# Performance work log

Measured on AMD Instinct MI355X. Metric: run time of the kernel, lower is better.

## Reference

```python
import jax, jax.numpy as jnp
import numpy as np

L, E, H, FF = 6, 768, 4, 3072
D = E // H
SCALE = float(E) ** -0.5  # note: source scales by embedding_size**-0.5, not head_dim
EPS = 1e-5


def layernorm(x, scale, bias):
    mu = jnp.mean(x, axis=-1, keepdims=True)
    var = jnp.mean((x - mu) ** 2, axis=-1, keepdims=True)
    return (x - mu) * jax.lax.rsqrt(var + EPS) * scale + bias


def setup_inputs() -> dict:
    key = jax.random.key(0)
    ks = jax.random.split(key, 16)
    s = 0.02
    inp = {
        "hidden_states": jax.random.normal(ks[0], (8, 1024, E), dtype=jnp.float32),
        "ln1_scale": jnp.ones((L, E), jnp.float32),
        "ln1_bias": jnp.zeros((L, E), jnp.float32),
        "wq": jax.random.normal(ks[1], (L, E, E), jnp.float32) * s,
        "wk": jax.random.normal(ks[2], (L, E, E), jnp.float32) * s,
        "wv": jax.random.normal(ks[3], (L, E, E), jnp.float32) * s,
        "wo": jax.random.normal(ks[4], (L, E, E), jnp.float32) * s,
        "bo": jnp.zeros((L, E), jnp.float32),
        "ln2_scale": jnp.ones((L, E), jnp.float32),
        "ln2_bias": jnp.zeros((L, E), jnp.float32),
        "w1": jax.random.normal(ks[5], (L, FF, E), jnp.float32) * s,
        "b1": jnp.zeros((L, FF), jnp.float32),
        "w2": jax.random.normal(ks[6], (L, E, FF), jnp.float32) * s,
        "b2": jnp.zeros((L, E), jnp.float32),
    }
    return inp


def _encoder(x, ln1_scale, ln1_bias, wq, wk, wv, wo, bo, ln2_scale, ln2_bias, w1, b1, w2, b2):
    B, S, _ = x.shape
    for i in range(L):
        h = layernorm(x, ln1_scale[i], ln1_bias[i])
        # torch Linear: y = x @ W.T
        q = (h @ wq[i].T).reshape(B, H, S, D)  # non-standard head split (reshape, no transpose) per source
        k = (h @ wk[i].T).reshape(B, H, S, D)
        v = (h @ wv[i].T).reshape(B, H, S, D)
        scores = jnp.einsum("bhsd,bhtd->bhst", q, k) * SCALE  # full SxS materialized, as in source
        attn = jax.nn.softmax(scores, axis=-1)
        o = jnp.einsum("bhst,bhtd->bhsd", attn, v)
        o = o.transpose(0, 2, 1, 3).reshape(B, S, E)
        x = x + (o @ wo[i].T + bo[i])
        h = layernorm(x, ln2_scale[i], ln2_bias[i])
        h = jax.nn.gelu(h @ w1[i].T + b1[i], approximate=False)  # nn.GELU default = exact erf
        x = x + (h @ w2[i].T + b2[i])  # dropout is identity in eval
    return x


def reference(hidden_states, ln1_scale, ln1_bias, wq, wk, wv, wo, bo, ln2_scale, ln2_bias, w1, b1, w2, b2):
    return _encoder(hidden_states, ln1_scale, ln1_bias, wq, wk, wv, wo, bo, ln2_scale, ln2_bias, w1, b1, w2, b2)
```

## Files before the change

kernel.cpp:

```cpp
#include <hip/hip_runtime.h>
#include <math.h>

typedef __attribute__((ext_vector_type(8))) __bf16 bf16x8;
typedef __attribute__((ext_vector_type(4))) __bf16 bf16x4;
typedef __attribute__((ext_vector_type(2))) __bf16 bf16x2;
typedef __attribute__((ext_vector_type(4))) float f32x4;

#define MFMA_BF16 __builtin_amdgcn_mfma_f32_16x16x32_bf16

constexpr int LAY = 6, E = 768, HH = 4, DH = 192, FF = 3072, BB = 8, SS = 1024, MM = 8192;
constexpr float ATT_SCALE = 0.03608439182435161f;

__device__ __forceinline__ void gl2lds16(const void* g, void* l) {
    __builtin_amdgcn_global_load_lds(
        (const __attribute__((address_space(1))) void*)g,
        (__attribute__((address_space(3))) void*)l, 16, 0, 0);
}

struct Cast6 {
    const float* src[6];
    __bf16* dst[6];
    int cum4[7];
};

__global__ __launch_bounds__(256) void cast6_kernel(Cast6 c, int total4) {
    int stride = gridDim.x * 256;
    for (int i = blockIdx.x * 256 + threadIdx.x; i < total4; i += stride) {
        int rgn = 0;
#pragma unroll
        for (int k = 1; k < 6; ++k) rgn += (i >= c.cum4[k]) ? 1 : 0;
        int off = i - c.cum4[rgn];
        f32x4 v = ((const f32x4*)c.src[rgn])[off];
        bf16x4 o;
        o[0] = (__bf16)v[0]; o[1] = (__bf16)v[1]; o[2] = (__bf16)v[2]; o[3] = (__bf16)v[3];
        ((bf16x4*)c.dst[rgn])[off] = o;
    }
}

__global__ __launch_bounds__(256) void ln_kernel(const float* __restrict__ x,
                                                 const float* __restrict__ gamma,
                                                 const float* __restrict__ beta,
                                                 __bf16* __restrict__ out) {
    size_t row = blockIdx.x;
    const float* xr = x + row * E;
    int t = threadIdx.x;
    float v0 = xr[t], v1 = xr[t + 256], v2 = xr[t + 512];
    float s = v0 + v1 + v2;
    float q = v0 * v0 + v1 * v1 + v2 * v2;
#pragma unroll
    for (int m = 1; m < 64; m <<= 1) { s += __shfl_xor(s, m); q += __shfl_xor(q, m); }
    __shared__ float red[8];
    int w = t >> 6;
    if ((t & 63) == 0) { red[w] = s; red[4 + w] = q; }
    __syncthreads();
    s = red[0] + red[1] + red[2] + red[3];
    q = red[4] + red[5] + red[6] + red[7];
    float mu = s * (1.0f / E);
    float var = q * (1.0f / E) - mu * mu;
    float rs = rsqrtf(var + 1e-5f);
    __bf16* orow = out + row * E;
    orow[t]       = (__bf16)((v0 - mu) * rs * gamma[t]       + beta[t]);
    orow[t + 256] = (__bf16)((v1 - mu) * rs * gamma[t + 256] + beta[t + 256]);
    orow[t + 512] = (__bf16)((v2 - mu) * rs * gamma[t + 512] + beta[t + 512]);
}

template <int EPI>
__global__ __launch_bounds__(256) void gemm_bt(
    const __bf16* __restrict__ A,
    const __bf16* __restrict__ B0, const __bf16* __restrict__ B1, const __bf16* __restrict__ B2,
    void* __restrict__ O0, void* __restrict__ O1, void* __restrict__ O2,
    const float* __restrict__ bias, int M, int N, int K) {
    __shared__ __bf16 smA[128 * 64];
    __shared__ __bf16 smB[128 * 64];
    int z = blockIdx.z;
    const __bf16* Bw = (z == 0) ? B0 : (z == 1) ? B1 : B2;
    void* Out = (z == 0) ? O0 : (z == 1) ? O1 : O2;
    int t = threadIdx.x;
    int w = t >> 6, lane = t & 63, b4 = lane >> 4, r = lane & 15;
    int mbase = blockIdx.y * 128, nbase = blockIdx.x * 128;
    int wm = (w >> 1) * 64, wn = (w & 1) * 64;
    const f32x4 fz = {0.f, 0.f, 0.f, 0.f};
    f32x4 acc[4][4];
#pragma unroll
    for (int a1 = 0; a1 < 4; ++a1)
#pragma unroll
        for (int a2 = 0; a2 < 4; ++a2) acc[a1][a2] = fz;
    const __bf16* Ap = A + (size_t)mbase * K;
    const __bf16* Bp = Bw + (size_t)nbase * K;
    int nk = K >> 6;
    for (int kt = 0; kt < nk; ++kt) {
        int k0 = kt * 64;
#pragma unroll
        for (int i = 0; i < 4; ++i) {
            int c = i * 256 + t;
            int row = c >> 3, ch = c & 7;
            int ldsoff = (i * 256 + w * 64) * 8;
            gl2lds16(Ap + (size_t)row * K + k0 + ch * 8, (void*)(smA + ldsoff));
            gl2lds16(Bp + (size_t)row * K + k0 + ch * 8, (void*)(smB + ldsoff));
        }
        __syncthreads();
#pragma unroll
        for (int ks = 0; ks < 2; ++ks) {
            bf16x8 af[4], bfr[4];
#pragma unroll
            for (int mi = 0; mi < 4; ++mi)
                af[mi] = *(const bf16x8*)(smA + (wm + mi * 16 + r) * 64 + ks * 32 + b4 * 8);
#pragma unroll
            for (int ni = 0; ni < 4; ++ni)
                bfr[ni] = *(const bf16x8*)(smB + (wn + ni * 16 + r) * 64 + ks * 32 + b4 * 8);
#pragma unroll
            for (int mi = 0; mi < 4; ++mi)
#pragma unroll
                for (int ni = 0; ni < 4; ++ni)
                    acc[mi][ni] = MFMA_BF16(af[mi], bfr[ni], acc[mi][ni], 0, 0, 0);
        }
        __syncthreads();
    }
#pragma unroll
    for (int mi = 0; mi < 4; ++mi) {
#pragma unroll
        for (int ni = 0; ni < 4; ++ni) {
            int col = nbase + wn + ni * 16 + r;
#pragma unroll
            for (int j = 0; j < 4; ++j) {
                int rowi = mbase + wm + mi * 16 + b4 * 4 + j;
                float v = acc[mi][ni][j];
                if constexpr (EPI == 0) {
                    ((__bf16*)Out)[(size_t)rowi * N + col] = (__bf16)v;
                } else if constexpr (EPI == 1) {
                    v += bias[col];
                    float g = 0.5f * v * (1.0f + erff(v * 0.70710678118654752f));
                    ((__bf16*)Out)[(size_t)rowi * N + col] = (__bf16)g;
                } else {
                    float* X = (float*)Out;
                    X[(size_t)rowi * N + col] += v + bias[col];
                }
            }
        }
    }
}

__global__ __launch_bounds__(256) void vtrans_kernel(const __bf16* __restrict__ v,
                                                     __bf16* __restrict__ vt) {
    __shared__ __bf16 tile[64 * 72];
    int bh = blockIdx.y;
    int si = blockIdx.x / 3, di = blockIdx.x % 3;
    int t = threadIdx.x;
    const __bf16* src = v + (size_t)bh * (SS * DH) + (size_t)(si * 64) * DH + di * 64;
#pragma unroll
    for (int i = 0; i < 2; ++i) {
        int c = i * 256 + t;
        int sl = c >> 3, dc = c & 7;
        *(bf16x8*)(tile + sl * 72 + dc * 8) = *(const bf16x8*)(src + (size_t)sl * DH + dc * 8);
    }
    __syncthreads();
    __bf16* dst = vt + ((size_t)bh * DH + di * 64) * SS + si * 64;
#pragma unroll
    for (int i = 0; i < 2; ++i) {
        int c = i * 256 + t;
        int dl = c >> 3, sc = c & 7;
        bf16x8 o;
#pragma unroll
        for (int e = 0; e < 8; ++e) o[e] = tile[(sc * 8 + e) * 72 + dl];
        *(bf16x8*)(dst + (size_t)dl * SS + sc * 8) = o;
    }
}

__global__ __launch_bounds__(256) void attn_kernel(const __bf16* __restrict__ qp,
                                                   const __bf16* __restrict__ kp,
                                                   const __bf16* __restrict__ vtp,
                                                   __bf16* __restrict__ ao) {
    __shared__ __bf16 smK[64 * 192];
    __shared__ __bf16 smVt[192 * 64];
    __shared__ __bf16 smP[4 * 16 * 72];
    int qt = blockIdx.x, h = blockIdx.y, b = blockIdx.z;
    int t = threadIdx.x, w = t >> 6, lane = t & 63, b4 = lane >> 4, r = lane & 15;
    size_t base = (size_t)b * (SS * E) + (size_t)h * (SS * DH);
    const __bf16* Q = qp + base;
    const __bf16* Kg = kp + base;
    const __bf16* VtG = vtp + (size_t)(b * HH + h) * DH * SS;
    int q0 = qt * 64 + w * 16;
    bf16x8 qf[6];
#pragma unroll
    for (int ks = 0; ks < 6; ++ks)
        qf[ks] = *(const bf16x8*)(Q + (size_t)(q0 + r) * DH + ks * 32 + b4 * 8);
    const f32x4 fz = {0.f, 0.f, 0.f, 0.f};
    f32x4 oacc[12];
#pragma unroll
    for (int i = 0; i < 12; ++i) oacc[i] = fz;
    float m_r[4], l_r[4];
#pragma unroll
    for (int j = 0; j < 4; ++j) { m_r[j] = -1e30f; l_r[j] = 0.f; }
    __bf16* smPw = smP + w * (16 * 72);

    for (int kt = 0; kt < 16; ++kt) {
        const __bf16* Ks = Kg + (size_t)kt * 64 * DH;
#pragma unroll
        for (int i = 0; i < 6; ++i) {
            int c = i * 256 + t;
            int row = c / 24, cc = c - row * 24;
            int scc = (cc & 0x18) | ((cc ^ row) & 7);
            gl2lds16(Ks + (size_t)row * DH + scc * 8,
                     (void*)(smK + (i * 256 + w * 64) * 8));
        }
#pragma unroll
        for (int i = 0; i < 6; ++i) {
            int c = i * 256 + t;
            int row = c >> 3, cc = c & 7;
            int scc = cc ^ (row & 7);
            gl2lds16(VtG + (size_t)row * SS + kt * 64 + scc * 8,
                     (void*)(smVt + (i * 256 + w * 64) * 8));
        }
        __syncthreads();
        f32x4 sc[4];
#pragma unroll
        for (int nt = 0; nt < 4; ++nt) sc[nt] = fz;
#pragma unroll
        for (int ks = 0; ks < 6; ++ks) {
#pragma unroll
            for (int nt = 0; nt < 4; ++nt) {
                int cc = ks * 4 + b4;
                int ccs = (cc & 0x18) | ((cc ^ r) & 7);
                bf16x8 kf = *(const bf16x8*)(smK + (nt * 16 + r) * 192 + ccs * 8);
                sc[nt] = MFMA_BF16(qf[ks], kf, sc[nt], 0, 0, 0);
            }
        }
#pragma unroll
        for (int nt = 0; nt < 4; ++nt) sc[nt] *= ATT_SCALE;
        float alpha[4];
#pragma unroll
        for (int j = 0; j < 4; ++j) {
            float mx = fmaxf(fmaxf(sc[0][j], sc[1][j]), fmaxf(sc[2][j], sc[3][j]));
#pragma unroll
            for (int msk = 1; msk < 16; msk <<= 1) mx = fmaxf(mx, __shfl_xor(mx, msk));
            float mn = fmaxf(m_r[j], mx);
            alpha[j] = __expf(m_r[j] - mn);
            m_r[j] = mn;
            float p0 = __expf(sc[0][j] - mn);
            float p1 = __expf(sc[1][j] - mn);
            float p2 = __expf(sc[2][j] - mn);
            float p3 = __expf(sc[3][j] - mn);
            sc[0][j] = p0; sc[1][j] = p1; sc[2][j] = p2; sc[3][j] = p3;
            float ps = p0 + p1 + p2 + p3;
#pragma unroll
            for (int msk = 1; msk < 16; msk <<= 1) ps += __shfl_xor(ps, msk);
            l_r[j] = l_r[j] * alpha[j] + ps;
        }
        {
            f32x4 a4 = {alpha[0], alpha[1], alpha[2], alpha[3]};
#pragma unroll
            for (int i = 0; i < 12; ++i) oacc[i] *= a4;
        }
#pragma unroll
        for (int nt = 0; nt < 4; ++nt)
#pragma unroll
            for (int j = 0; j < 4; ++j)
                smPw[(b4 * 4 + j) * 72 + nt * 16 + r] = (__bf16)sc[nt][j];
        __asm__ volatile("s_waitcnt lgkmcnt(0)" ::: "memory");
#pragma unroll
        for (int kt2 = 0; kt2 < 2; ++kt2) {
            bf16x8 pa = *(const bf16x8*)(smPw + r * 72 + kt2 * 32 + b4 * 8);
#pragma unroll
            for (int nt = 0; nt < 12; ++nt) {
                int ccs = (kt2 * 4 + b4) ^ (r & 7);
                bf16x8 vf = *(const bf16x8*)(smVt + (nt * 16 + r) * 64 + ccs * 8);
                oacc[nt] = MFMA_BF16(pa, vf, oacc[nt], 0, 0, 0);
            }
        }
        __syncthreads();
    }
    float inv[4];
#pragma unroll
    for (int j = 0; j < 4; ++j) inv[j] = 1.0f / l_r[j];
    __bf16* obase = ao + (size_t)b * (SS * E);
#pragma unroll
    for (int nt = 0; nt < 12; ++nt)
#pragma unroll
        for (int j = 0; j < 4; ++j) {
            int srow = q0 + b4 * 4 + j;
            obase[(size_t)srow * E + h * DH + nt * 16 + r] = (__bf16)(oacc[nt][j] * inv[j]);
        }
}

extern "C" void kernel_launch(void* const* d_in, const int* in_sizes, int n_in,
                              void* d_out, int out_size, void* d_ws, size_t ws_size,
                              hipStream_t stream) {
    const float* hs   = (const float*)d_in[0];
    const float* ln1s = (const float*)d_in[1];
    const float* ln1b = (const float*)d_in[2];
    const float* wq   = (const float*)d_in[3];
    const float* wk   = (const float*)d_in[4];
    const float* wv   = (const float*)d_in[5];
    const float* wo   = (const float*)d_in[6];
    const float* bo   = (const float*)d_in[7];
    const float* ln2s = (const float*)d_in[8];
    const float* ln2b = (const float*)d_in[9];
    const float* w1   = (const float*)d_in[10];
    const float* b1   = (const float*)d_in[11];
    const float* w2   = (const float*)d_in[12];
    const float* b2   = (const float*)d_in[13];
    float* X = (float*)d_out;

    char* ws = (char*)d_ws;
    size_t off = 0;
    auto alloc = [&](size_t bytes) {
        char* p = ws + off;
        off += (bytes + 255) & ~(size_t)255;
        return p;
    };
    __bf16* wq_b = (__bf16*)alloc((size_t)E * E * 2);
    __bf16* wk_b = (__bf16*)alloc((size_t)E * E * 2);
    __bf16* wv_b = (__bf16*)alloc((size_t)E * E * 2);
    __bf16* wo_b = (__bf16*)alloc((size_t)E * E * 2);
    __bf16* w1_b = (__bf16*)alloc((size_t)FF * E * 2);
    __bf16* w2_b = (__bf16*)alloc((size_t)FF * E * 2);
    __bf16* h_b  = (__bf16*)alloc((size_t)MM * E * 2);
    char* U = alloc((size_t)MM * FF * 2);
    const size_t SLOT = (size_t)MM * E * 2;
    __bf16* q_b  = (__bf16*)U;
    __bf16* k_b  = (__bf16*)(U + SLOT);
    __bf16* v_b  = (__bf16*)(U + 2 * SLOT);
    __bf16* vt_b = (__bf16*)(U + 3 * SLOT);
    __bf16* a_b  = (__bf16*)(U + 2 * SLOT);
    __bf16* f_b  = (__bf16*)U;

    hipMemcpyAsync(d_out, hs, (size_t)MM * E * 4, hipMemcpyDeviceToDevice, stream);

    for (int i = 0; i < LAY; ++i) {
        Cast6 c;
        c.src[0] = wq + (size_t)i * E * E;  c.dst[0] = wq_b;
        c.src[1] = wk + (size_t)i * E * E;  c.dst[1] = wk_b;
        c.src[2] = wv + (size_t)i * E * E;  c.dst[2] = wv_b;
        c.src[3] = wo + (size_t)i * E * E;  c.dst[3] = wo_b;
        c.src[4] = w1 + (size_t)i * FF * E; c.dst[4] = w1_b;
        c.src[5] = w2 + (size_t)i * FF * E; c.dst[5] = w2_b;
        int n4[6] = {E * E / 4, E * E / 4, E * E / 4, E * E / 4, FF * E / 4, FF * E / 4};
        c.cum4[0] = 0;
        for (int k = 0; k < 6; ++k) c.cum4[k + 1] = c.cum4[k] + n4[k];
        int total4 = c.cum4[6];
        cast6_kernel<<<1024, 256, 0, stream>>>(c, total4);

        ln_kernel<<<MM, 256, 0, stream>>>(X, ln1s + (size_t)i * E, ln1b + (size_t)i * E, h_b);

        gemm_bt<0><<<dim3(E / 128, MM / 128, 3), 256, 0, stream>>>(
            h_b, wq_b, wk_b, wv_b, q_b, k_b, v_b, nullptr, MM, E, E);

        vtrans_kernel<<<dim3(48, 32), 256, 0, stream>>>(v_b, vt_b);

        attn_kernel<<<dim3(SS / 64, HH, BB), 256, 0, stream>>>(q_b, k_b, vt_b, a_b);

        gemm_bt<2><<<dim3(E / 128, MM / 128, 1), 256, 0, stream>>>(
            a_b, wo_b, wo_b, wo_b, X, X, X, bo + (size_t)i * E, MM, E, E);

        ln_kernel<<<MM, 256, 0, stream>>>(X, ln2s + (size_t)i * E, ln2b + (size_t)i * E, h_b);

        gemm_bt<1><<<dim3(FF / 128, MM / 128, 1), 256, 0, stream>>>(
            h_b, w1_b, w1_b, w1_b, f_b, f_b, f_b, b1 + (size_t)i * FF, MM, FF, E);

        gemm_bt<2><<<dim3(E / 128, MM / 128, 1), 256, 0, stream>>>(
            f_b, w2_b, w2_b, w2_b, X, X, X, b2 + (size_t)i * E, MM, E, FF);
    }
}
```

Measured before the change: 2.158 ms.

## Replace 128x128 GEMM with 256x256 multi-stage pipelined MFMA kernel

The GEMM kernel now uses 256x256 output tiles with 512 threads and a 4-slot LDS ring buffer filled by async global-to-LDS loads, with explicit vmcnt waits. This replaces the single-buffered load/sync/compute loop. It also adds an XOR swizzle on LDS columns to avoid bank conflicts, remaps block IDs so neighbouring tiles land together, and raises MFMA priority with s_setprio. The larger tiles sharply cut the block count for the N=768 GEMMs, to 96 blocks for the Wo and W2 projections, which can leave many compute units idle.

```diff
diff --git a/kernel.cpp b/kernel.cpp
--- a/kernel.cpp
+++ b/kernel.cpp
@@ -65,65 +65,108 @@
 }
 
 template <int EPI>
-__global__ __launch_bounds__(256) void gemm_bt(
+__global__ __launch_bounds__(512, 2) void gemm256(
     const __bf16* __restrict__ A,
     const __bf16* __restrict__ B0, const __bf16* __restrict__ B1, const __bf16* __restrict__ B2,
     void* __restrict__ O0, void* __restrict__ O1, void* __restrict__ O2,
     const float* __restrict__ bias, int M, int N, int K) {
-    __shared__ __bf16 smA[128 * 64];
-    __shared__ __bf16 smB[128 * 64];
+    __shared__ __bf16 lds[4 * 16384];
     int z = blockIdx.z;
     const __bf16* Bw = (z == 0) ? B0 : (z == 1) ? B1 : B2;
     void* Out = (z == 0) ? O0 : (z == 1) ? O1 : O2;
     int t = threadIdx.x;
     int w = t >> 6, lane = t & 63, b4 = lane >> 4, r = lane & 15;
-    int mbase = blockIdx.y * 128, nbase = blockIdx.x * 128;
-    int wm = (w >> 1) * 64, wn = (w & 1) * 64;
+    int gx = gridDim.x;
+    int nwg = gx * gridDim.y;
+    int bid = blockIdx.y * gx + blockIdx.x;
+    int cpx = nwg >> 3;
+    int swz = (bid & 7) * cpx + (bid >> 3);
+    int bx = swz % gx, by = swz / gx;
+    int mbase = by * 256, nbase = bx * 256;
+    int wr = w >> 2, wc = w & 3;
     const f32x4 fz = {0.f, 0.f, 0.f, 0.f};
-    f32x4 acc[4][4];
-#pragma unroll
-    for (int a1 = 0; a1 < 4; ++a1)
+    f32x4 acc[8][4];
+#pragma unroll
+    for (int a1 = 0; a1 < 8; ++a1)
 #pragma unroll
         for (int a2 = 0; a2 < 4; ++a2) acc[a1][a2] = fz;
     const __bf16* Ap = A + (size_t)mbase * K;
     const __bf16* Bp = Bw + (size_t)nbase * K;
-    int nk = K >> 6;
-    for (int kt = 0; kt < nk; ++kt) {
-        int k0 = kt * 64;
-#pragma unroll
-        for (int i = 0; i < 4; ++i) {
-            int c = i * 256 + t;
-            int row = c >> 3, ch = c & 7;
-            int ldsoff = (i * 256 + w * 64) * 8;
-            gl2lds16(Ap + (size_t)row * K + k0 + ch * 8, (void*)(smA + ldsoff));
-            gl2lds16(Bp + (size_t)row * K + k0 + ch * 8, (void*)(smB + ldsoff));
-        }
-        __syncthreads();
-#pragma unroll
-        for (int ks = 0; ks < 2; ++ks) {
-            bf16x8 af[4], bfr[4];
-#pragma unroll
-            for (int mi = 0; mi < 4; ++mi)
-                af[mi] = *(const bf16x8*)(smA + (wm + mi * 16 + r) * 64 + ks * 32 + b4 * 8);
+    int nk = K >> 5;
+
+    auto stageA = [&](int tt) {
+        int slot = (tt & 3) * 16384;
+        int k0 = tt * 32;
+#pragma unroll
+        for (int i = 0; i < 2; ++i) {
+            int c = i * 512 + t;
+            int row = c >> 2, cl = c & 3;
+            int sc = cl ^ ((row >> 1) & 3);
+            gl2lds16(Ap + (size_t)row * K + k0 + sc * 8,
+                     (void*)(lds + slot + (i * 512 + w * 64) * 8));
+        }
+    };
+    auto stageB = [&](int tt) {
+        int slot = (tt & 3) * 16384 + 8192;
+        int k0 = tt * 32;
+#pragma unroll
+        for (int i = 0; i < 2; ++i) {
+            int c = i * 512 + t;
+            int row = c >> 2, cl = c & 3;
+            int sc = cl ^ ((row >> 1) & 3);
+            gl2lds16(Bp + (size_t)row * K + k0 + sc * 8,
+                     (void*)(lds + slot + (i * 512 + w * 64) * 8));
+        }
+    };
+
+    int swch = (b4 ^ ((r >> 1) & 3)) * 8;
+    int aoff = (wr * 128 + r) * 32 + swch;
+    int boff = (wc * 64 + r) * 32 + swch;
+
+    stageA(0); stageB(0); stageA(1); stageB(1); stageA(2); stageB(2);
+
+    for (int tt = 0; tt < nk; ++tt) {
+        if (tt < nk - 2)       asm volatile("s_waitcnt vmcnt(8)" ::: "memory");
+        else if (tt == nk - 2) asm volatile("s_waitcnt vmcnt(4)" ::: "memory");
+        else                   asm volatile("s_waitcnt vmcnt(0)" ::: "memory");
+        __builtin_amdgcn_s_barrier();
+        asm volatile("" ::: "memory");
+        const __bf16* sa = lds + (tt & 3) * 16384;
+        const __bf16* sb = sa + 8192;
+        bool do_stage = (tt + 3) < nk;
+        bf16x8 bfr[4], af[4];
+#pragma unroll
+        for (int ni = 0; ni < 4; ++ni) bfr[ni] = *(const bf16x8*)(sb + boff + ni * 512);
+#pragma unroll
+        for (int mi = 0; mi < 4; ++mi) af[mi] = *(const bf16x8*)(sa + aoff + mi * 512);
+        if (do_stage) stageA(tt + 3);
+        __builtin_amdgcn_s_setprio(1);
+#pragma unroll
+        for (int mi = 0; mi < 4; ++mi)
 #pragma unroll
             for (int ni = 0; ni < 4; ++ni)
-                bfr[ni] = *(const bf16x8*)(smB + (wn + ni * 16 + r) * 64 + ks * 32 + b4 * 8);
-#pragma unroll
-            for (int mi = 0; mi < 4; ++mi)
-#pragma unroll
-                for (int ni = 0; ni < 4; ++ni)
-                    acc[mi][ni] = MFMA_BF16(af[mi], bfr[ni], acc[mi][ni], 0, 0, 0);
-        }
-        __syncthreads();
-    }
-#pragma unroll
-    for (int mi = 0; mi < 4; ++mi) {
+                acc[mi][ni] = MFMA_BF16(af[mi], bfr[ni], acc[mi][ni], 0, 0, 0);
+        __builtin_amdgcn_s_setprio(0);
+#pragma unroll
+        for (int mi = 0; mi < 4; ++mi) af[mi] = *(const bf16x8*)(sa + aoff + (mi + 4) * 512);
+        if (do_stage) stageB(tt + 3);
+        __builtin_amdgcn_s_setprio(1);
+#pragma unroll
+        for (int mi = 0; mi < 4; ++mi)
+#pragma unroll
+            for (int ni = 0; ni < 4; ++ni)
+                acc[mi + 4][ni] = MFMA_BF16(af[mi], bfr[ni], acc[mi + 4][ni], 0, 0, 0);
+        __builtin_amdgcn_s_setprio(0);
+    }
+
+#pragma unroll
+    for (int mi = 0; mi < 8; ++mi) {
 #pragma unroll
         for (int ni = 0; ni < 4; ++ni) {
-            int col = nbase + wn + ni * 16 + r;
+            int col = nbase + wc * 64 + ni * 16 + r;
 #pragma unroll
             for (int j = 0; j < 4; ++j) {
-                int rowi = mbase + wm + mi * 16 + b4 * 4 + j;
+                int rowi = mbase + wr * 128 + mi * 16 + b4 * 4 + j;
                 float v = acc[mi][ni][j];
                 if constexpr (EPI == 0) {
                     ((__bf16*)Out)[(size_t)rowi * N + col] = (__bf16)v;
@@ -342,22 +385,22 @@
 
         ln_kernel<<<MM, 256, 0, stream>>>(X, ln1s + (size_t)i * E, ln1b + (size_t)i * E, h_b);
 
-        gemm_bt<0><<<dim3(E / 128, MM / 128, 3), 256, 0, stream>>>(
+        gemm256<0><<<dim3(E / 256, MM / 256, 3), 512, 0, stream>>>(
             h_b, wq_b, wk_b, wv_b, q_b, k_b, v_b, nullptr, MM, E, E);
 
         vtrans_kernel<<<dim3(48, 32), 256, 0, stream>>>(v_b, vt_b);
 
         attn_kernel<<<dim3(SS / 64, HH, BB), 256, 0, stream>>>(q_b, k_b, vt_b, a_b);
 
-        gemm_bt<2><<<dim3(E / 128, MM / 128, 1), 256, 0, stream>>>(
+        gemm256<2><<<dim3(E / 256, MM / 256, 1), 512, 0, stream>>>(
             a_b, wo_b, wo_b, wo_b, X, X, X, bo + (size_t)i * E, MM, E, E);
 
         ln_kernel<<<MM, 256, 0, stream>>>(X, ln2s + (size_t)i * E, ln2b + (size_t)i * E, h_b);
 
-        gemm_bt<1><<<dim3(FF / 128, MM / 128, 1), 256, 0, stream>>>(
+        gemm256<1><<<dim3(FF / 256, MM / 256, 1), 512, 0, stream>>>(
             h_b, w1_b, w1_b, w1_b, f_b, f_b, f_b, b1 + (size_t)i * FF, MM, FF, E);
 
-        gemm_bt<2><<<dim3(E / 128, MM / 128, 1), 256, 0, stream>>>(
+        gemm256<2><<<dim3(E / 256, MM / 256, 1), 512, 0, stream>>>(
             f_b, w2_b, w2_b, w2_b, X, X, X, b2 + (size_t)i * E, MM, E, FF);
     }
 }
```

Result: no change. 2.121 ms (-1.8%).

## Add LDS XOR swizzle, block swizzle, and split-K with atomics to GEMMs

Applied to the files above, without the earlier changes.

The GEMM kernel now XOR-swizzles the 16-byte chunks written to LDS so the MFMA fragment reads avoid bank conflicts. It remaps block IDs across groups of eight for better L2 locality and sets launch bounds to 4 waves per SIMD. The residual-add GEMMs (Wo and W2) now use split-K=2 with float atomicAdd into X, adding bias only in the first split. This raises parallelism for the N=768 outputs, at the cost of atomic traffic and non-deterministic summation order.

```diff
diff --git a/kernel.cpp b/kernel.cpp
--- a/kernel.cpp
+++ b/kernel.cpp
@@ -64,50 +64,79 @@
     orow[t + 512] = (__bf16)((v2 - mu) * rs * gamma[t + 512] + beta[t + 512]);
 }
 
-template <int EPI>
-__global__ __launch_bounds__(256) void gemm_bt(
+template <int EPI, int SPLITK>
+__global__ __launch_bounds__(256, 4) void gemm128(
     const __bf16* __restrict__ A,
     const __bf16* __restrict__ B0, const __bf16* __restrict__ B1, const __bf16* __restrict__ B2,
     void* __restrict__ O0, void* __restrict__ O1, void* __restrict__ O2,
     const float* __restrict__ bias, int M, int N, int K) {
-    __shared__ __bf16 smA[128 * 64];
-    __shared__ __bf16 smB[128 * 64];
+    __shared__ __bf16 lds[2 * 8192];
     int z = blockIdx.z;
-    const __bf16* Bw = (z == 0) ? B0 : (z == 1) ? B1 : B2;
-    void* Out = (z == 0) ? O0 : (z == 1) ? O1 : O2;
+    const __bf16* Bw;
+    void* Out;
+    int ksp;
+    if constexpr (SPLITK > 1) {
+        Bw = B0; Out = O0; ksp = z;
+    } else {
+        Bw = (z == 0) ? B0 : (z == 1) ? B1 : B2;
+        Out = (z == 0) ? O0 : (z == 1) ? O1 : O2;
+        ksp = 0;
+    }
+    int Keff = K / SPLITK;
     int t = threadIdx.x;
     int w = t >> 6, lane = t & 63, b4 = lane >> 4, r = lane & 15;
-    int mbase = blockIdx.y * 128, nbase = blockIdx.x * 128;
-    int wm = (w >> 1) * 64, wn = (w & 1) * 64;
+    int gx = gridDim.x;
+    int nwg = gx * gridDim.y;
+    int bid = blockIdx.y * gx + blockIdx.x;
+    int cpx = nwg >> 3;
+    int swz = (bid & 7) * cpx + (bid >> 3);
+    int bx = swz % gx, by = swz / gx;
+    int mbase = by * 128, nbase = bx * 128;
+    int wr = w >> 1, wc = w & 1;
     const f32x4 fz = {0.f, 0.f, 0.f, 0.f};
     f32x4 acc[4][4];
 #pragma unroll
     for (int a1 = 0; a1 < 4; ++a1)
 #pragma unroll
         for (int a2 = 0; a2 < 4; ++a2) acc[a1][a2] = fz;
-    const __bf16* Ap = A + (size_t)mbase * K;
-    const __bf16* Bp = Bw + (size_t)nbase * K;
-    int nk = K >> 6;
+    const __bf16* Ap = A + (size_t)mbase * K + ksp * Keff;
+    const __bf16* Bp = Bw + (size_t)nbase * K + ksp * Keff;
+    int nk = Keff >> 6;
+
+    const __bf16* sA[4];
+    const __bf16* sB[4];
+#pragma unroll
+    for (int i = 0; i < 4; ++i) {
+        int c = i * 256 + t;
+        int row = c >> 3;
+        int col = ((c ^ row) & 7) * 8;
+        sA[i] = Ap + (size_t)row * K + col;
+        sB[i] = Bp + (size_t)row * K + col;
+    }
+
+    int ch0 = ((b4) ^ (r & 7)) * 8;
+    int ch1 = ((4 + b4) ^ (r & 7)) * 8;
+    int arow = (wr * 64 + r) * 64;
+    int brow = 8192 + (wc * 64 + r) * 64;
+
     for (int kt = 0; kt < nk; ++kt) {
-        int k0 = kt * 64;
 #pragma unroll
         for (int i = 0; i < 4; ++i) {
-            int c = i * 256 + t;
-            int row = c >> 3, ch = c & 7;
-            int ldsoff = (i * 256 + w * 64) * 8;
-            gl2lds16(Ap + (size_t)row * K + k0 + ch * 8, (void*)(smA + ldsoff));
-            gl2lds16(Bp + (size_t)row * K + k0 + ch * 8, (void*)(smB + ldsoff));
+            gl2lds16(sA[i], (void*)(lds + i * 2048 + w * 512));
+            gl2lds16(sB[i], (void*)(lds + 8192 + i * 2048 + w * 512));
+            sA[i] += 64; sB[i] += 64;
         }
         __syncthreads();
 #pragma unroll
         for (int ks = 0; ks < 2; ++ks) {
+            int chk = ks ? ch1 : ch0;
             bf16x8 af[4], bfr[4];
 #pragma unroll
             for (int mi = 0; mi < 4; ++mi)
-                af[mi] = *(const bf16x8*)(smA + (wm + mi * 16 + r) * 64 + ks * 32 + b4 * 8);
+                af[mi] = *(const bf16x8*)(lds + arow + mi * 1024 + chk);
 #pragma unroll
             for (int ni = 0; ni < 4; ++ni)
-                bfr[ni] = *(const bf16x8*)(smB + (wn + ni * 16 + r) * 64 + ks * 32 + b4 * 8);
+                bfr[ni] = *(const bf16x8*)(lds + brow + ni * 1024 + chk);
 #pragma unroll
             for (int mi = 0; mi < 4; ++mi)
 #pragma unroll
@@ -116,14 +145,15 @@
         }
         __syncthreads();
     }
+
 #pragma unroll
     for (int mi = 0; mi < 4; ++mi) {
 #pragma unroll
         for (int ni = 0; ni < 4; ++ni) {
-            int col = nbase + wn + ni * 16 + r;
+            int col = nbase + wc * 64 + ni * 16 + r;
 #pragma unroll
             for (int j = 0; j < 4; ++j) {
-                int rowi = mbase + wm + mi * 16 + b4 * 4 + j;
+                int rowi = mbase + wr * 64 + mi * 16 + b4 * 4 + j;
                 float v = acc[mi][ni][j];
                 if constexpr (EPI == 0) {
                     ((__bf16*)Out)[(size_t)rowi * N + col] = (__bf16)v;
@@ -133,7 +163,8 @@
                     ((__bf16*)Out)[(size_t)rowi * N + col] = (__bf16)g;
                 } else {
                     float* X = (float*)Out;
-                    X[(size_t)rowi * N + col] += v + bias[col];
+                    float add = v + (ksp == 0 ? bias[col] : 0.0f);
+                    atomicAdd(&X[(size_t)rowi * N + col], add);
                 }
             }
         }
@@ -342,22 +373,22 @@
 
         ln_kernel<<<MM, 256, 0, stream>>>(X, ln1s + (size_t)i * E, ln1b + (size_t)i * E, h_b);
 
-        gemm_bt<0><<<dim3(E / 128, MM / 128, 3), 256, 0, stream>>>(
+        gemm128<0, 1><<<dim3(E / 128, MM / 128, 3), 256, 0, stream>>>(
             h_b, wq_b, wk_b, wv_b, q_b, k_b, v_b, nullptr, MM, E, E);
 
         vtrans_kernel<<<dim3(48, 32), 256, 0, stream>>>(v_b, vt_b);
 
         attn_kernel<<<dim3(SS / 64, HH, BB), 256, 0, stream>>>(q_b, k_b, vt_b, a_b);
 
-        gemm_bt<2><<<dim3(E / 128, MM / 128, 1), 256, 0, stream>>>(
+        gemm128<2, 2><<<dim3(E / 128, MM / 128, 2), 256, 0, stream>>>(
             a_b, wo_b, wo_b, wo_b, X, X, X, bo + (size_t)i * E, MM, E, E);
 
         ln_kernel<<<MM, 256, 0, stream>>>(X, ln2s + (size_t)i * E, ln2b + (size_t)i * E, h_b);
 
-        gemm_bt<1><<<dim3(FF / 128, MM / 128, 1), 256, 0, stream>>>(
+        gemm128<1, 1><<<dim3(FF / 128, MM / 128, 1), 256, 0, stream>>>(
             h_b, w1_b, w1_b, w1_b, f_b, f_b, f_b, b1 + (size_t)i * FF, MM, FF, E);
 
-        gemm_bt<2><<<dim3(E / 128, MM / 128, 1), 256, 0, stream>>>(
+        gemm128<2, 2><<<dim3(E / 128, MM / 128, 2), 256, 0, stream>>>(
             f_b, w2_b, w2_b, w2_b, X, X, X, b2 + (size_t)i * E, MM, E, FF);
     }
 }
```

Result: faster. 1.778 ms (-17.6%).
